# Kernel tuning notes

Measured on AMD Instinct MI355X. Metric: run time of the kernel, lower is better.

The kernel has to match this reference:

```python
import jax, jax.numpy as jnp
import numpy as np

B, T, D, H, HS = 2, 256, 2048, 32, 64
LORA, DLORA, ST = 32, 64, 66  # maa lora rank, decay lora rank, state rows (2+HS)
EPS = 1e-5


def setup_inputs() -> dict:
    key = jax.random.key(0)
    ks = jax.random.split(key, 24)
    n = lambda k, sh, s=0.02: (jax.random.normal(k, sh, jnp.float32) * s)
    u = lambda k, sh: jax.random.uniform(k, sh, jnp.float32)
    return {
        "x": jax.random.normal(ks[0], (B, T, D), jnp.float32),
        "state": jax.random.normal(ks[1], (B, ST, D), jnp.float32) * 0.1,
        "ln1_w": jnp.ones((D,), jnp.float32),
        "ln1_b": jnp.zeros((D,), jnp.float32),
        "time_maa_x": u(ks[2], (D,)),
        "time_maa_w1": n(ks[3], (D, 5 * LORA)),
        "time_maa_w2": n(ks[4], (5, LORA, D)),
        "time_maa_k": u(ks[5], (D,)),
        "time_maa_w": u(ks[6], (D,)),
        "time_maa_v": u(ks[7], (D,)),
        "time_maa_r": u(ks[8], (D,)),
        "time_maa_g": u(ks[9], (D,)),
        "time_decay": n(ks[10], (D,), 0.5),
        "time_decay_w1": n(ks[11], (D, DLORA)),
        "time_decay_w2": n(ks[12], (DLORA, D)),
        "time_faaaa": n(ks[13], (H, HS, 1), 0.1),
        "receptance_weight": n(ks[14], (D, D)),
        "key_weight": n(ks[15], (D, D)),
        "value_weight": n(ks[16], (D, D)),
        "output_weight": n(ks[17], (D, D)),
        "gate_weight": n(ks[18], (D, D)),
        "lnx_w": jnp.ones((D,), jnp.float32),
        "lnx_b": jnp.zeros((D,), jnp.float32),
        "i": 0,
    }


def reference(x, state, ln1_w, ln1_b, time_maa_x, time_maa_w1, time_maa_w2,
              time_maa_k, time_maa_w, time_maa_v, time_maa_r, time_maa_g,
              time_decay, time_decay_w1, time_decay_w2, time_faaaa,
              receptance_weight, key_weight, value_weight, output_weight,
              gate_weight, lnx_w, lnx_b, i):
    # forward() early-returns time_mixing(ln1(x), state, i)
    mu = x.mean(-1, keepdims=True)
    var = ((x - mu) ** 2).mean(-1, keepdims=True)
    x = (x - mu) * jax.lax.rsqrt(var + EPS) * ln1_w + ln1_b

    i1 = (2 + HS) * i + 1
    # token shift: sx[t] = x[t-1] - x[t], with state row i1 as x[-1]
    sx = jnp.concatenate([state[:, i1][:, None] - x[:, :1], x[:, :-1] - x[:, 1:]], axis=1)

    xxx = x + sx * time_maa_x
    t5 = jnp.tanh(xxx @ time_maa_w1).reshape(B, T, 5, LORA)
    xxx5 = jnp.einsum('btfr,frd->btfd', t5, time_maa_w2)          # [B,T,5,D]
    maa = jnp.stack([time_maa_k, time_maa_w, time_maa_v, time_maa_r, time_maa_g])  # [5,D]
    x5 = x[:, :, None] + sx[:, :, None] * (maa + xxx5)            # [B,T,5,D]

    k = (x5[:, :, 0] @ key_weight.T).reshape(B, T, H, HS)
    w = jnp.exp(-jnp.exp(time_decay + jnp.tanh(x5[:, :, 1] @ time_decay_w1) @ time_decay_w2)).reshape(B, T, H, HS)
    v = (x5[:, :, 2] @ value_weight.T).reshape(B, T, H, HS)
    r = (x5[:, :, 3] @ receptance_weight.T).reshape(B, T, H, HS)
    g = jax.nn.silu(x5[:, :, 4] @ gate_weight.T)                  # [B,T,D]

    kv = jnp.einsum('bthi,bthj->bthij', k, v)                     # [B,T,H,HS,HS]
    prev0 = state[:, i1 + 1:i1 + 1 + HS].reshape(B, H, HS, HS)

    def step(prev, xs):
        kv_t, w_t = xs
        return kv_t + w_t[..., None] * prev, prev  # emit state BEFORE update

    _, state_s = jax.lax.scan(step, prev0,
                              (kv.transpose(1, 0, 2, 3, 4), w.transpose(1, 0, 2, 3)))
    state_s = state_s.transpose(1, 0, 2, 3, 4)                    # [B,T,H,HS,HS]

    wkv = time_faaaa * kv + state_s
    rwkv = jnp.einsum('bthj,bthjd->bthd', r, wkv)                 # [B,T,H,HS]

    # GroupNorm(num_groups=H) over each head's HS channels
    gm = rwkv.mean(-1, keepdims=True)
    gv = ((rwkv - gm) ** 2).mean(-1, keepdims=True)
    normed = (rwkv - gm) * jax.lax.rsqrt(gv + EPS)
    normed = normed * lnx_w.reshape(H, HS) + lnx_b.reshape(H, HS)
    normed = normed.reshape(B, T, D)

    return (normed * g) @ output_weight.T
```

## Files before the change

kernel.cpp:

```cpp
#include <hip/hip_runtime.h>
#include <hip/hip_bf16.h>

typedef unsigned short u16;
typedef __attribute__((ext_vector_type(4))) float f32x4;
typedef __attribute__((ext_vector_type(8))) short short8;
typedef __attribute__((ext_vector_type(4))) short bf16x4;

#define B_ 2
#define T_ 256
#define D_ 2048
#define H_ 32
#define HS_ 64
#define M_ 512
#define ST_ 66
#define EPS_ 1e-5f
#define NC_ 16
#define CL_ 16

__device__ __forceinline__ float bf2f(u16 u) {
    union { unsigned int i; float f; } c; c.i = ((unsigned int)u) << 16; return c.f;
}
__device__ __forceinline__ u16 f2bf(float f) {
    union { unsigned int i; float f; } c; c.f = f;
    unsigned int r = c.i + 0x7fffu + ((c.i >> 16) & 1u);
    return (u16)(r >> 16);
}
__device__ __forceinline__ u16 f2bf_hw(float f) {
    __hip_bfloat16 b = __float2bfloat16(f);
    return *reinterpret_cast<u16*>(&b);
}

__device__ __forceinline__ void gld16(const u16* g, u16* l) {
    __builtin_amdgcn_global_load_lds((const __attribute__((address_space(1))) void*)g,
                                     (__attribute__((address_space(3))) void*)l, 16, 0, 0);
}

__global__ __launch_bounds__(256) void ln_kernel(const float* __restrict__ x, const float* __restrict__ w,
                                                 const float* __restrict__ bias, float* __restrict__ xln)
{
    const int row = blockIdx.x;
    const float* xr = x + (size_t)row * D_;
    float* orow = xln + (size_t)row * D_;
    const int t = threadIdx.x;
    f32x4 a0 = *(const f32x4*)(xr + t * 8);
    f32x4 a1 = *(const f32x4*)(xr + t * 8 + 4);
    float s = 0.f, q = 0.f;
#pragma unroll
    for (int i = 0; i < 4; i++) { s += a0[i] + a1[i]; q += a0[i]*a0[i] + a1[i]*a1[i]; }
#pragma unroll
    for (int off = 1; off < 64; off <<= 1) { s += __shfl_xor(s, off, 64); q += __shfl_xor(q, off, 64); }
    __shared__ float ls[4], lq[4];
    const int wid = t >> 6, lane = t & 63;
    if (lane == 0) { ls[wid] = s; lq[wid] = q; }
    __syncthreads();
    s = ls[0] + ls[1] + ls[2] + ls[3];
    q = lq[0] + lq[1] + lq[2] + lq[3];
    const float mu = s * (1.f / D_);
    const float var = q * (1.f / D_) - mu * mu;
    const float rs = rsqrtf(var + EPS_);
#pragma unroll
    for (int i = 0; i < 8; i++) {
        int d = t * 8 + i;
        float f = (i < 4) ? a0[i] : a1[i - 4];
        orow[d] = (f - mu) * rs * w[d] + bias[d];
    }
}

__global__ __launch_bounds__(256) void shift_kernel(const float* __restrict__ xln, const float* __restrict__ state,
                                                    const float* __restrict__ maax, const int* __restrict__ ip,
                                                    float* __restrict__ sx, u16* __restrict__ xxxb)
{
    const size_t gid = (size_t)blockIdx.x * 256 + threadIdx.x;
    const size_t e = gid * 4;
    const int row = (int)(e >> 11);
    const int d = (int)(e & 2047);
    const int tt = row & (T_ - 1);
    const int b = row >> 8;
    const float* prev;
    if (tt == 0) prev = state + ((size_t)b * ST_ + (size_t)(66 * ip[0] + 1)) * D_ + d;
    else         prev = xln + e - D_;
    f32x4 p = *(const f32x4*)prev;
    f32x4 c = *(const f32x4*)(xln + e);
    f32x4 mx = *(const f32x4*)(maax + d);
    f32x4 sv;
    bf16x4 xv;
#pragma unroll
    for (int i = 0; i < 4; i++) { sv[i] = p[i] - c[i]; xv[i] = (short)f2bf(c[i] + sv[i] * mx[i]); }
    *(f32x4*)(sx + e) = sv;
    *(bf16x4*)(xxxb + e) = xv;
}

__global__ __launch_bounds__(256) void txp_kernel(const float* __restrict__ in, u16* __restrict__ out,
                                                  int K, int N)
{
    __shared__ float tile[32][33];
    const int k0 = blockIdx.x * 32, n0 = blockIdx.y * 32;
    const int c = threadIdx.x & 31, r8 = threadIdx.x >> 5;
#pragma unroll
    for (int i = 0; i < 4; i++) {
        int r = r8 + i * 8;
        tile[r][c] = in[(size_t)(k0 + r) * N + (n0 + c)];
    }
    __syncthreads();
#pragma unroll
    for (int i = 0; i < 4; i++) {
        int r = r8 + i * 8;
        out[(size_t)(n0 + r) * K + (k0 + c)] = f2bf(tile[c][r]);
    }
}

template<bool TANH>
__global__ __launch_bounds__(512) void wdot_kernel(const u16* __restrict__ A, const u16* __restrict__ Wt,
                                                   float* __restrict__ C, int N)
{
    const int gw = (int)((blockIdx.x * 512 + threadIdx.x) >> 6);
    const int lane = threadIdx.x & 63;
    const int m = gw / N, n = gw - m * N;
    const u16* a = A + (size_t)m * D_ + lane * 8;
    const u16* w = Wt + (size_t)n * D_ + lane * 8;
    float acc = 0.f;
#pragma unroll
    for (int i = 0; i < 4; i++) {
        short8 av = *(const short8*)(a + i * 512);
        short8 wv = *(const short8*)(w + i * 512);
#pragma unroll
        for (int j = 0; j < 8; j++)
            acc = fmaf(bf2f((u16)av[j]), bf2f((u16)wv[j]), acc);
    }
#pragma unroll
    for (int off = 1; off < 64; off <<= 1) acc += __shfl_xor(acc, off, 64);
    if (lane == 0) C[gw] = TANH ? tanhf(acc) : acc;
}

__global__ __launch_bounds__(256) void maa2_kernel(const float* __restrict__ t5, const float* __restrict__ w2,
                                                   const float* __restrict__ xln, const float* __restrict__ sxp,
                                                   const float* __restrict__ mk, const float* __restrict__ mw,
                                                   const float* __restrict__ mv, const float* __restrict__ mr,
                                                   const float* __restrict__ mg, u16* __restrict__ x5)
{
    const int gid = blockIdx.x * 256 + threadIdx.x;
    const int d = gid & (D_ - 1);
    const int mg4 = gid >> 11;
    const size_t m0 = (size_t)mg4 * 4;
    float xl[4], sv[4];
#pragma unroll
    for (int mm = 0; mm < 4; mm++) {
        const size_t e = (m0 + mm) * D_ + d;
        xl[mm] = xln[e];
        sv[mm] = sxp[e];
    }
    const float* t5b = t5 + m0 * 160;
#pragma unroll
    for (int f = 0; f < 5; f++) {
        const float* maa = (f == 0) ? mk : (f == 1) ? mw : (f == 2) ? mv : (f == 3) ? mr : mg;
        const float mf = maa[d];
        const float* w2f = w2 + (size_t)f * 32 * D_ + d;
        float a0 = 0, a1 = 0, a2 = 0, a3 = 0;
#pragma unroll 8
        for (int r = 0; r < 32; r++) {
            const float wv = w2f[(size_t)r * D_];
            a0 = fmaf(t5b[f * 32 + r], wv, a0);
            a1 = fmaf(t5b[160 + f * 32 + r], wv, a1);
            a2 = fmaf(t5b[320 + f * 32 + r], wv, a2);
            a3 = fmaf(t5b[480 + f * 32 + r], wv, a3);
        }
        const float accs[4] = {a0, a1, a2, a3};
#pragma unroll
        for (int mm = 0; mm < 4; mm++) {
            const size_t e = (m0 + mm) * D_ + d;
            x5[(size_t)f * M_ * D_ + e] = f2bf(xl[mm] + sv[mm] * (mf + accs[mm]));
        }
    }
}

__global__ __launch_bounds__(256) void decay2_kernel(const float* __restrict__ td, const float* __restrict__ dw2,
                                                     const float* __restrict__ tdec, float* __restrict__ wout)
{
    const int gid = blockIdx.x * 256 + threadIdx.x;
    const int d = gid & (D_ - 1);
    const int mg4 = gid >> 11;
    const float* wp = dw2 + d;
    const float* tb = td + (size_t)mg4 * 4 * 64;
    float a0 = 0, a1 = 0, a2 = 0, a3 = 0;
#pragma unroll 8
    for (int r = 0; r < 64; r++) {
        float wv = wp[(size_t)r * D_];
        a0 = fmaf(tb[r], wv, a0);
        a1 = fmaf(tb[64 + r], wv, a1);
        a2 = fmaf(tb[128 + r], wv, a2);
        a3 = fmaf(tb[192 + r], wv, a3);
    }
    const float base = tdec[d];
    const float accs[4] = {a0, a1, a2, a3};
#pragma unroll
    for (int mm = 0; mm < 4; mm++)
        wout[((size_t)mg4 * 4 + mm) * D_ + d] = expf(-expf(base + accs[mm]));
}

__device__ __forceinline__ void gemm2p_body(const u16* __restrict__ A, const float* __restrict__ Wf,
                                            float* __restrict__ C, int m0, int n0, int k0, int KC)
{
    __shared__ u16 As[2][128 * 64];
    __shared__ u16 Bs[2][64 * 64];
    const int tid = threadIdx.x;
    const int lane = tid & 63;
    const int wvd = tid >> 6;
    const int wm = (wvd >> 1) * 64;
    const int wn = (wvd & 1) * 32;

    f32x4 acc[4][2];
#pragma unroll
    for (int i = 0; i < 4; i++)
#pragma unroll
        for (int j = 0; j < 2; j++) { acc[i][j][0]=0.f; acc[i][j][1]=0.f; acc[i][j][2]=0.f; acc[i][j][3]=0.f; }

    const int srow = tid >> 3;
    const int sw8  = (((tid & 7) ^ (srow & 7)) << 3);
    const u16* Ag = A + (size_t)(m0 + srow) * D_ + k0 + sw8;
    const int ldst = tid * 8;

    const int br  = tid >> 2;
    const int bc0 = (tid & 3) * 16;
    const float* Wg = Wf + (size_t)(n0 + br) * D_ + k0 + bc0;
    const int bb0 = bc0 >> 3;
    const int dst0 = br * 64 + ((bb0 ^ (br & 7)) << 3);
    const int dst1 = br * 64 + (((bb0 + 1) ^ (br & 7)) << 3);

    const int rsw = (lane & 7) << 3;
    const int colb = (lane >> 4) * 8;
    const int fr = lane & 15;

    f32x4 bl0, bl1, bl2, bl3;
#define LOADB_(kt) { bl0 = *(const f32x4*)(Wg + (kt));      bl1 = *(const f32x4*)(Wg + (kt) + 4);  \
                     bl2 = *(const f32x4*)(Wg + (kt) + 8);  bl3 = *(const f32x4*)(Wg + (kt) + 12); }
#define STAGEA_(bb, kt)                                                           \
    {                                                                             \
        _Pragma("unroll")                                                         \
        for (int i = 0; i < 4; i++)                                               \
            gld16(Ag + (size_t)(i * 32) * D_ + (kt), &As[bb][i * 2048 + ldst]);   \
    }
#define WRITEB_(bb)                                                               \
    {                                                                             \
        short8 p0, p1;                                                            \
        _Pragma("unroll")                                                         \
        for (int j = 0; j < 4; j++) {                                             \
            p0[j]     = (short)f2bf_hw(bl0[j]); p0[j + 4] = (short)f2bf_hw(bl1[j]); \
            p1[j]     = (short)f2bf_hw(bl2[j]); p1[j + 4] = (short)f2bf_hw(bl3[j]); \
        }                                                                         \
        *(short8*)&Bs[bb][dst0] = p0;                                             \
        *(short8*)&Bs[bb][dst1] = p1;                                             \
    }

    LOADB_(0);
    STAGEA_(0, 0);
    WRITEB_(0);
    __syncthreads();
    int cur = 0;
    for (int kt = 0; kt < KC; kt += 64) {
        const bool more = kt + 64 < KC;
        if (more) { LOADB_(kt + 64); STAGEA_(cur ^ 1, kt + 64); }
#pragma unroll
        for (int kk = 0; kk < 64; kk += 32) {
            const int c = (kk + colb) ^ rsw;
            short8 av[4], bv[2];
#pragma unroll
            for (int mi = 0; mi < 4; mi++)
                av[mi] = *(const short8*)&As[cur][(wm + mi * 16 + fr) * 64 + c];
#pragma unroll
            for (int ni = 0; ni < 2; ni++)
                bv[ni] = *(const short8*)&Bs[cur][(wn + ni * 16 + fr) * 64 + c];
#pragma unroll
            for (int mi = 0; mi < 4; mi++)
#pragma unroll
                for (int ni = 0; ni < 2; ni++)
                    acc[mi][ni] = __builtin_amdgcn_mfma_f32_16x16x32_bf16(av[mi], bv[ni], acc[mi][ni], 0, 0, 0);
        }
        if (more) WRITEB_(cur ^ 1);
        __syncthreads();
        cur ^= 1;
    }
#undef LOADB_
#undef STAGEA_
#undef WRITEB_
    const int cr = wm + (lane >> 4) * 4;
    const int cc = wn + fr;
#pragma unroll
    for (int mi = 0; mi < 4; mi++)
#pragma unroll
        for (int ni = 0; ni < 2; ni++)
#pragma unroll
            for (int j = 0; j < 4; j++)
                C[(size_t)(m0 + cr + mi * 16 + j) * D_ + (n0 + cc + ni * 16)] = acc[mi][ni][j];
}

__global__ __launch_bounds__(256) void gemm4g_kernel(const u16* __restrict__ x5, const float* __restrict__ Wk,
                                                     const float* __restrict__ Wv, const float* __restrict__ Wr,
                                                     const float* __restrict__ Wg, float* __restrict__ kvK,
                                                     float* __restrict__ kvV, float* __restrict__ kvR,
                                                     float* __restrict__ kvG)
{
    const int s = blockIdx.z;
    const u16* A = x5 + (size_t)(s == 0 ? 0 : s + 1) * M_ * D_;
    const float* W = (s == 0) ? Wk : (s == 1) ? Wv : (s == 2) ? Wr : Wg;
    float* C = (s == 0) ? kvK : (s == 1) ? kvV : (s == 2) ? kvR : kvG;
    gemm2p_body(A, W, C, blockIdx.y * 128, blockIdx.x * 64, 0, D_);
}

__global__ __launch_bounds__(256) void gemm1g_kernel(const u16* __restrict__ y, const float* __restrict__ wo,
                                                     float* __restrict__ out, float* __restrict__ p0,
                                                     float* __restrict__ p1, float* __restrict__ p2)
{
    const int ks = blockIdx.z;
    float* C = (ks == 0) ? out : (ks == 1) ? p0 : (ks == 2) ? p1 : p2;
    gemm2p_body(y, wo, C, blockIdx.y * 128, blockIdx.x * 64, ks * 512, 512);
}

__global__ __launch_bounds__(256) void add3_kernel(float* __restrict__ dst, const float* __restrict__ s0,
                                                   const float* __restrict__ s1, const float* __restrict__ s2)
{
    const size_t e = ((size_t)blockIdx.x * 256 + threadIdx.x) * 4;
    f32x4 d = *(const f32x4*)(dst + e);
    f32x4 a = *(const f32x4*)(s0 + e);
    f32x4 b = *(const f32x4*)(s1 + e);
    f32x4 c = *(const f32x4*)(s2 + e);
#pragma unroll
    for (int i = 0; i < 4; i++) d[i] += (a[i] + b[i]) + c[i];
    *(f32x4*)(dst + e) = d;
}

__global__ __launch_bounds__(512) void rec1_kernel(const float* __restrict__ rB, const float* __restrict__ kB,
                                                   const float* __restrict__ wB, const float* __restrict__ vB,
                                                   const float* __restrict__ fa, float* __restrict__ rwkv,
                                                   float* __restrict__ CS, float* __restrict__ RP,
                                                   float* __restrict__ PC)
{
    const int bx = blockIdx.x;
    const int c  = bx & (NC_ - 1);
    const int bh = bx >> 4;
    const int h = bh & 31, b = bh >> 5;
    const int tid = threadIdx.x;
    const int wv = tid >> 6, lane = tid & 63;
    const int wg = wv >> 2;
    const int jb = lane >> 3, dsub = lane & 7;
    const int jbase = jb * 8;
    const int d0 = wg * 32 + (wv & 3) * 8 + dsub;

    __shared__ float stage[4][CL_][64];
    __shared__ float p2[CL_][8][64];
    __shared__ float p1[CL_][8];
    __shared__ float rpS[CL_ * 64];

    float S[8], pv[8], faj[8];
#pragma unroll
    for (int q = 0; q < 8; q++) { S[q] = 0.f; pv[q] = 1.f; faj[q] = fa[h * 64 + jbase + q]; }

    const size_t base = ((size_t)b * T_ * H_ + h) * HS_;
    const int t0 = c * CL_;
    const int arr = wv & 3;
    const float* mysrc = (arr == 0) ? rB : (arr == 1) ? kB : (arr == 2) ? wB : vB;
    const int ts0 = wg * 8 + (lane >> 4);
    const int sch = (lane & 15) * 4;
    const bool p1w = (wv == 0 && dsub == 0);

#pragma unroll
    for (int p = 0; p < 2; p++) {
        f32x4 v = *(const f32x4*)(mysrc + base + (size_t)(t0 + ts0 + p * 4) * (H_ * HS_) + sch);
        *(f32x4*)&stage[arr][ts0 + p * 4][sch] = v;
    }
    __syncthreads();

    f32x4 r0 = *(const f32x4*)&stage[0][0][jbase];
    f32x4 r1 = *(const f32x4*)&stage[0][0][jbase + 4];
    f32x4 k0 = *(const f32x4*)&stage[1][0][jbase];
    f32x4 k1 = *(const f32x4*)&stage[1][0][jbase + 4];
    f32x4 w0 = *(const f32x4*)&stage[2][0][jbase];
    f32x4 w1 = *(const f32x4*)&stage[2][0][jbase + 4];
    float vd = stage[3][0][d0];
#pragma unroll
    for (int ts = 0; ts < CL_; ++ts) {
        f32x4 nr0 = r0, nr1 = r1, nk0 = k0, nk1 = k1, nw0 = w0, nw1 = w1;
        float nvd = vd;
        if (ts + 1 < CL_) {
            nr0 = *(const f32x4*)&stage[0][ts + 1][jbase];
            nr1 = *(const f32x4*)&stage[0][ts + 1][jbase + 4];
            nk0 = *(const f32x4*)&stage[1][ts + 1][jbase];
            nk1 = *(const f32x4*)&stage[1][ts + 1][jbase + 4];
            nw0 = *(const f32x4*)&stage[2][ts + 1][jbase];
            nw1 = *(const f32x4*)&stage[2][ts + 1][jbase + 4];
            nvd = stage[3][ts + 1][d0];
        }
        float s1 = 0.f, s2 = 0.f;
#pragma unroll
        for (int q = 0; q < 4; q++) {
            s1 = fmaf(r0[q] * faj[q],     k0[q], s1);
            s1 = fmaf(r1[q] * faj[q + 4], k1[q], s1);
            s2 = fmaf(r0[q], S[q],     s2);
            s2 = fmaf(r1[q], S[q + 4], s2);
        }
        p2[ts][jb][d0 ^ (jb << 3)] = s2;
        if (p1w) {
            p1[ts][jb] = s1;
#pragma unroll
            for (int q = 0; q < 4; q++) {
                rpS[ts * 64 + jbase + q]     = r0[q] * pv[q];
                rpS[ts * 64 + jbase + 4 + q] = r1[q] * pv[q + 4];
            }
        }
#pragma unroll
        for (int q = 0; q < 4; q++) {
            pv[q]     *= w0[q];
            pv[q + 4] *= w1[q];
            S[q]       = fmaf(w0[q], S[q],     k0[q] * vd);
            S[q + 4]   = fmaf(w1[q], S[q + 4], k1[q] * vd);
        }
        r0 = nr0; r1 = nr1; k0 = nk0; k1 = nk1; w0 = nw0; w1 = nw1; vd = nvd;
    }
    __syncthreads();
#pragma unroll
    for (int p = 0; p < 2; p++) {
        const int ts = wv * 2 + p;
        f32x4 p1a = *(const f32x4*)&p1[ts][0];
        f32x4 p1b = *(const f32x4*)&p1[ts][4];
        float s1t = ((p1a[0] + p1a[1]) + (p1a[2] + p1a[3])) +
                    ((p1b[0] + p1b[1]) + (p1b[2] + p1b[3]));
        float s2t = 0.f;
#pragma unroll
        for (int j = 0; j < 8; j++) s2t += p2[ts][j][lane ^ (j << 3)];
        const float vvv = stage[3][ts][lane];
        rwkv[base + (size_t)(t0 + ts) * (H_ * HS_) + lane] = fmaf(vvv, s1t, s2t);
    }
    RP[(size_t)bx * (CL_ * 64) + tid]       = rpS[tid];
    RP[(size_t)bx * (CL_ * 64) + 512 + tid] = rpS[512 + tid];
#pragma unroll
    for (int q = 0; q < 8; q++)
        CS[(size_t)bx * 4096 + (size_t)(jbase + q) * 64 + d0] = S[q];
    if (p1w) {
#pragma unroll
        for (int q = 0; q < 8; q++)
            PC[(size_t)bx * 64 + jbase + q] = pv[q];
    }
}

__global__ __launch_bounds__(512) void rec2_kernel(const float* __restrict__ state, const int* __restrict__ ip,
                                                   float* __restrict__ CS, const float* __restrict__ PC)
{
    const int bh = blockIdx.x;
    const int b = bh >> 5, h = bh & 31;
    const int tid = threadIdx.x;
    const int o = tid * 8;
    const int jrow = tid >> 3;
    const float* Sp = state + (size_t)b * ST_ * D_ + (size_t)(66 * ip[0] + 2) * D_ + (size_t)h * HS_ * HS_;
    f32x4 c0 = *(const f32x4*)(Sp + o);
    f32x4 c1 = *(const f32x4*)(Sp + o + 4);
    for (int c = 0; c < NC_; ++c) {
        float* cs = CS + ((size_t)(bh * NC_ + c)) * 4096 + o;
        f32x4 l0 = *(const f32x4*)cs;
        f32x4 l1 = *(const f32x4*)(cs + 4);
        const float pc = PC[(size_t)(bh * NC_ + c) * 64 + jrow];
        f32x4 n0, n1;
#pragma unroll
        for (int i = 0; i < 4; i++) { n0[i] = fmaf(pc, c0[i], l0[i]); n1[i] = fmaf(pc, c1[i], l1[i]); }
        *(f32x4*)cs = c0;
        *(f32x4*)(cs + 4) = c1;
        c0 = n0; c1 = n1;
    }
}

__global__ __launch_bounds__(256) void rec3gn_kernel(const float* __restrict__ CS, const float* __restrict__ RP,
                                                     const float* __restrict__ rwkv, const float* __restrict__ gpre,
                                                     const float* __restrict__ lnxw, const float* __restrict__ lnxb,
                                                     u16* __restrict__ y)
{
    const int bx = blockIdx.x;
    const int c  = bx & (NC_ - 1);
    const int bh = bx >> 4;
    const int h = bh & 31, b = bh >> 5;
    const int tid = threadIdx.x;
    __shared__ float Ss[4096];
    __shared__ float rp[CL_ * 64];
#pragma unroll
    for (int i = 0; i < 4; i++)
        *(f32x4*)&Ss[tid * 4 + i * 1024] = *(const f32x4*)(CS + (size_t)bx * 4096 + tid * 4 + i * 1024);
    *(f32x4*)&rp[tid * 4] = *(const f32x4*)(RP + (size_t)bx * (CL_ * 64) + tid * 4);
    __syncthreads();
    const int tl = tid >> 4;
    const int d4 = (tid & 15) * 4;
    f32x4 acc; acc[0] = acc[1] = acc[2] = acc[3] = 0.f;
    const float* rpr = &rp[tl * 64];
#pragma unroll 16
    for (int j = 0; j < 64; ++j) {
        const float rv = rpr[j];
        const f32x4 sv = *(const f32x4*)&Ss[j * 64 + d4];
#pragma unroll
        for (int i = 0; i < 4; i++) acc[i] = fmaf(rv, sv[i], acc[i]);
    }
    const size_t base = ((size_t)b * T_ * H_ + h) * HS_;
    const size_t eb = base + (size_t)(c * CL_ + tl) * (H_ * HS_);
    const f32x4 cur = *(const f32x4*)(rwkv + eb + d4);
    f32x4 val;
#pragma unroll
    for (int i = 0; i < 4; i++) val[i] = cur[i] + acc[i];
    float s = 0.f, q = 0.f;
#pragma unroll
    for (int i = 0; i < 4; i++) { s += val[i]; q += val[i] * val[i]; }
#pragma unroll
    for (int off = 1; off < 16; off <<= 1) { s += __shfl_xor(s, off, 64); q += __shfl_xor(q, off, 64); }
    const float mu = s * (1.f / 64.f);
    const float var = q * (1.f / 64.f) - mu * mu;
    const float rs = rsqrtf(var + EPS_);
    bf16x4 yv;
#pragma unroll
    for (int i = 0; i < 4; i++) {
        const int hj = h * 64 + d4 + i;
        const float nrm = (val[i] - mu) * rs * lnxw[hj] + lnxb[hj];
        const float gp = gpre[eb + d4 + i];
        const float gv = gp / (1.f + expf(-gp));
        yv[i] = (short)f2bf(nrm * gv);
    }
    *(bf16x4*)(y + eb + d4) = yv;
}

extern "C" void kernel_launch(void* const* d_in, const int* in_sizes, int n_in,
                              void* d_out, int out_size, void* d_ws, size_t ws_size,
                              hipStream_t stream)
{
    const float* x     = (const float*)d_in[0];
    const float* state = (const float*)d_in[1];
    const float* ln1w  = (const float*)d_in[2];
    const float* ln1b  = (const float*)d_in[3];
    const float* maax  = (const float*)d_in[4];
    const float* w1    = (const float*)d_in[5];
    const float* w2    = (const float*)d_in[6];
    const float* maak  = (const float*)d_in[7];
    const float* maaw  = (const float*)d_in[8];
    const float* maav  = (const float*)d_in[9];
    const float* maar  = (const float*)d_in[10];
    const float* maag  = (const float*)d_in[11];
    const float* tdec  = (const float*)d_in[12];
    const float* dw1   = (const float*)d_in[13];
    const float* dw2   = (const float*)d_in[14];
    const float* fa    = (const float*)d_in[15];
    const float* wrec  = (const float*)d_in[16];
    const float* wkey  = (const float*)d_in[17];
    const float* wval  = (const float*)d_in[18];
    const float* wout  = (const float*)d_in[19];
    const float* wgate = (const float*)d_in[20];
    const float* lnxw  = (const float*)d_in[21];
    const float* lnxb  = (const float*)d_in[22];
    const int*   ip    = (const int*)d_in[23];

    char* ws = (char*)d_ws;
    const size_t MD = (size_t)M_ * D_;
    float* CS   = (float*)(ws);
    float* RP   = (float*)(ws + ((size_t)16 << 20));
    float* PC   = (float*)(ws + ((size_t)20 << 20));
    float* xln  = (float*)(ws + ((size_t)40 << 20));
    float* sx   = (float*)(ws + ((size_t)44 << 20));
    u16*   xxxb = (u16*)  (ws + ((size_t)48 << 20));
    u16*   w1t  = (u16*)  (ws + ((size_t)50 << 20));
    u16*   dw1t = (u16*)  (ws + ((size_t)51 << 20));
    float* t5   = (float*)(ws + ((size_t)52 << 20));
    float* td   = (float*)(ws + ((size_t)53 << 20));
    u16*   x5   = (u16*)  (ws + ((size_t)54 << 20));
    float* wdec = (float*)(ws + ((size_t)64 << 20));
    float* kvK  = (float*)(ws + ((size_t)40 << 20));
    float* kvV  = (float*)(ws + ((size_t)44 << 20));
    float* kvR  = (float*)(ws + ((size_t)48 << 20));
    float* kvG  = (float*)(ws + ((size_t)68 << 20));
    float* rwkv = (float*)(ws + ((size_t)72 << 20));
    u16*   y    = (u16*)  (ws + ((size_t)76 << 20));
    float* pp0  = (float*)(ws + ((size_t)54 << 20));
    float* pp1  = (float*)(ws + ((size_t)58 << 20));
    float* pp2  = (float*)(ws + ((size_t)62 << 20));
    float* out  = (float*)d_out;

    hipLaunchKernelGGL(ln_kernel,     dim3(512),      dim3(256), 0, stream, x, ln1w, ln1b, xln);
    hipLaunchKernelGGL(shift_kernel,  dim3(1024),     dim3(256), 0, stream, xln, state, maax, ip, sx, xxxb);
    hipLaunchKernelGGL(txp_kernel,    dim3(64, 5),    dim3(256), 0, stream, w1, w1t, D_, 160);
    hipLaunchKernelGGL(txp_kernel,    dim3(64, 2),    dim3(256), 0, stream, dw1, dw1t, D_, 64);
    hipLaunchKernelGGL((wdot_kernel<true>), dim3(10240), dim3(512), 0, stream, xxxb, w1t, t5, 160);
    hipLaunchKernelGGL(maa2_kernel,   dim3(1024),     dim3(256), 0, stream, t5, w2, xln, sx, maak, maaw, maav, maar, maag, x5);
    hipLaunchKernelGGL((wdot_kernel<true>), dim3(4096), dim3(512), 0, stream, x5 + MD, dw1t, td, 64);
    hipLaunchKernelGGL(decay2_kernel, dim3(1024),     dim3(256), 0, stream, td, dw2, tdec, wdec);
    hipLaunchKernelGGL(gemm4g_kernel, dim3(32, 4, 4), dim3(256), 0, stream, x5, wkey, wval, wrec, wgate, kvK, kvV, kvR, kvG);
    hipLaunchKernelGGL(rec1_kernel,   dim3(B_ * H_ * NC_), dim3(512), 0, stream, kvR, kvK, wdec, kvV, fa, rwkv, CS, RP, PC);
    hipLaunchKernelGGL(rec2_kernel,   dim3(B_ * H_),  dim3(512), 0, stream, state, ip, CS, PC);
    hipLaunchKernelGGL(rec3gn_kernel, dim3(B_ * H_ * NC_), dim3(256), 0, stream, CS, RP, rwkv, kvG, lnxw, lnxb, y);
    hipLaunchKernelGGL(gemm1g_kernel, dim3(32, 4, 4), dim3(256), 0, stream, y, wout, out, pp0, pp1, pp2);
    hipLaunchKernelGGL(add3_kernel,   dim3(1024),     dim3(256), 0, stream, out, pp0, pp1, pp2);

    (void)in_sizes; (void)n_in; (void)out_size; (void)ws_size;
}
```

Before: 183.7 us.

## Restructure GEMM main loop into manually unrolled ping-pong pipeline with explicit waitcnts

```diff
diff --git a/kernel.cpp b/kernel.cpp
--- a/kernel.cpp
+++ b/kernel.cpp
@@ -230,58 +230,83 @@
     const int colb = (lane >> 4) * 8;
     const int fr = lane & 15;
 
-    f32x4 bl0, bl1, bl2, bl3;
-#define LOADB_(kt) { bl0 = *(const f32x4*)(Wg + (kt));      bl1 = *(const f32x4*)(Wg + (kt) + 4);  \
-                     bl2 = *(const f32x4*)(Wg + (kt) + 8);  bl3 = *(const f32x4*)(Wg + (kt) + 12); }
+    f32x4 xa0, xa1, xa2, xa3;
+    f32x4 xb0, xb1, xb2, xb3;
+
+#define LOADB_A(kt) { xa0 = *(const f32x4*)(Wg + (kt));      xa1 = *(const f32x4*)(Wg + (kt) + 4);  \
+                      xa2 = *(const f32x4*)(Wg + (kt) + 8);  xa3 = *(const f32x4*)(Wg + (kt) + 12); }
+#define LOADB_B(kt) { xb0 = *(const f32x4*)(Wg + (kt));      xb1 = *(const f32x4*)(Wg + (kt) + 4);  \
+                      xb2 = *(const f32x4*)(Wg + (kt) + 8);  xb3 = *(const f32x4*)(Wg + (kt) + 12); }
 #define STAGEA_(bb, kt)                                                           \
     {                                                                             \
         _Pragma("unroll")                                                         \
         for (int i = 0; i < 4; i++)                                               \
             gld16(Ag + (size_t)(i * 32) * D_ + (kt), &As[bb][i * 2048 + ldst]);   \
     }
-#define WRITEB_(bb)                                                               \
+#define WRITEB_(bb, r0, r1, r2, r3)                                               \
     {                                                                             \
         short8 p0, p1;                                                            \
         _Pragma("unroll")                                                         \
         for (int j = 0; j < 4; j++) {                                             \
-            p0[j]     = (short)f2bf_hw(bl0[j]); p0[j + 4] = (short)f2bf_hw(bl1[j]); \
-            p1[j]     = (short)f2bf_hw(bl2[j]); p1[j + 4] = (short)f2bf_hw(bl3[j]); \
+            p0[j]     = (short)f2bf_hw(r0[j]); p0[j + 4] = (short)f2bf_hw(r1[j]); \
+            p1[j]     = (short)f2bf_hw(r2[j]); p1[j + 4] = (short)f2bf_hw(r3[j]); \
         }                                                                         \
         *(short8*)&Bs[bb][dst0] = p0;                                             \
         *(short8*)&Bs[bb][dst1] = p1;                                             \
     }
-
-    LOADB_(0);
+#define MFMA_(bb)                                                                 \
+    {                                                                             \
+        _Pragma("unroll")                                                         \
+        for (int kk = 0; kk < 64; kk += 32) {                                     \
+            const int c = (kk + colb) ^ rsw;                                      \
+            short8 av[4], bv[2];                                                  \
+            _Pragma("unroll")                                                     \
+            for (int mi = 0; mi < 4; mi++)                                        \
+                av[mi] = *(const short8*)&As[bb][(wm + mi * 16 + fr) * 64 + c];   \
+            _Pragma("unroll")                                                     \
+            for (int ni = 0; ni < 2; ni++)                                        \
+                bv[ni] = *(const short8*)&Bs[bb][(wn + ni * 16 + fr) * 64 + c];   \
+            _Pragma("unroll")                                                     \
+            for (int mi = 0; mi < 4; mi++)                                        \
+                _Pragma("unroll")                                                 \
+                for (int ni = 0; ni < 2; ni++)                                    \
+                    acc[mi][ni] = __builtin_amdgcn_mfma_f32_16x16x32_bf16(av[mi], bv[ni], acc[mi][ni], 0, 0, 0); \
+        }                                                                         \
+    }
+
+    LOADB_A(0);
     STAGEA_(0, 0);
-    WRITEB_(0);
-    __syncthreads();
-    int cur = 0;
-    for (int kt = 0; kt < KC; kt += 64) {
-        const bool more = kt + 64 < KC;
-        if (more) { LOADB_(kt + 64); STAGEA_(cur ^ 1, kt + 64); }
-#pragma unroll
-        for (int kk = 0; kk < 64; kk += 32) {
-            const int c = (kk + colb) ^ rsw;
-            short8 av[4], bv[2];
-#pragma unroll
-            for (int mi = 0; mi < 4; mi++)
-                av[mi] = *(const short8*)&As[cur][(wm + mi * 16 + fr) * 64 + c];
-#pragma unroll
-            for (int ni = 0; ni < 2; ni++)
-                bv[ni] = *(const short8*)&Bs[cur][(wn + ni * 16 + fr) * 64 + c];
-#pragma unroll
-            for (int mi = 0; mi < 4; mi++)
-#pragma unroll
-                for (int ni = 0; ni < 2; ni++)
-                    acc[mi][ni] = __builtin_amdgcn_mfma_f32_16x16x32_bf16(av[mi], bv[ni], acc[mi][ni], 0, 0, 0);
-        }
-        if (more) WRITEB_(cur ^ 1);
-        __syncthreads();
-        cur ^= 1;
-    }
-#undef LOADB_
+    for (int kt = 0; ; kt += 128) {
+        {
+            const bool m1 = kt + 64 < KC;
+            if (m1) { LOADB_B(kt + 64); STAGEA_(1, kt + 64); }
+            if (m1) asm volatile("s_waitcnt vmcnt(8)" ::: "memory");
+            else    asm volatile("s_waitcnt vmcnt(0)" ::: "memory");
+            WRITEB_(0, xa0, xa1, xa2, xa3);
+            asm volatile("s_waitcnt lgkmcnt(0)" ::: "memory");
+            __builtin_amdgcn_s_barrier();
+            MFMA_(0);
+            __builtin_amdgcn_s_barrier();
+            if (!m1) break;
+        }
+        {
+            const bool m2 = kt + 128 < KC;
+            if (m2) { LOADB_A(kt + 128); STAGEA_(0, kt + 128); }
+            if (m2) asm volatile("s_waitcnt vmcnt(8)" ::: "memory");
+            else    asm volatile("s_waitcnt vmcnt(0)" ::: "memory");
+            WRITEB_(1, xb0, xb1, xb2, xb3);
+            asm volatile("s_waitcnt lgkmcnt(0)" ::: "memory");
+            __builtin_amdgcn_s_barrier();
+            MFMA_(1);
+            __builtin_amdgcn_s_barrier();
+            if (!m2) break;
+        }
+    }
+#undef LOADB_A
+#undef LOADB_B
 #undef STAGEA_
 #undef WRITEB_
+#undef MFMA_
     const int cr = wm + (lane >> 4) * 4;
     const int cc = wn + fr;
 #pragma unroll
```

Result: no change. 182.4 us (-0.7%).
